# Kernel optimization log

Measured on AMD Instinct MI355X. Metric: run time of the kernel, lower is better.

Reference implementation:

```python
import jax, jax.numpy as jnp
import numpy as np

ORDER = 32


def setup_inputs() -> dict:
    key = jax.random.key(0)
    ks = jax.random.split(key, 12)
    S, N, W, OUT = 2048, 100000, ORDER * ORDER, 4 * ORDER * ORDER
    sc = lambda fan_in: 1.0 / np.sqrt(fan_in)
    return {
        "sources": jax.random.normal(ks[0], (S, 4), jnp.float32),
        "r": jax.random.normal(ks[1], (N, 2), jnp.float32),
        "W1": jax.random.normal(ks[2], (W, 4), jnp.float32) * sc(4),
        "b1": jax.random.normal(ks[3], (W,), jnp.float32) * 0.01,
        "W2": jax.random.normal(ks[4], (W, W), jnp.float32) * sc(W),
        "b2": jax.random.normal(ks[5], (W,), jnp.float32) * 0.01,
        "W3": jax.random.normal(ks[6], (W, W), jnp.float32) * sc(W),
        "b3": jax.random.normal(ks[7], (W,), jnp.float32) * 0.01,
        "W4": jax.random.normal(ks[8], (OUT, W), jnp.float32) * sc(W),
        "b4": jax.random.normal(ks[9], (OUT,), jnp.float32) * 0.01,
        "Wb": jax.random.normal(ks[10], (4,), jnp.float32) * sc(4),
        "bb": jax.random.normal(ks[11], (), jnp.float32) * 0.01,
    }


def reference(sources, r, W1, b1, W2, b2, W3, b3, W4, b4, Wb, bb):
    order = ORDER
    # hypermodel MLP (vmapped over sources == batched matmuls)
    h = jax.nn.gelu(sources @ W1.T + b1)
    h = jax.nn.gelu(h @ W2.T + b2)
    h = jax.nn.gelu(h @ W3.T + b3)
    w = h @ W4.T + b4                       # (S, 4*order^2)
    b = sources @ Wb + bb                   # (S,) scalar bias per source
    # prepare_weights: sum over sources
    wsum = jnp.sum(w, axis=0).reshape(4, order, order)
    bsum = jnp.sum(b)
    # fourier_expansion: sum_{c,i,j} w[c,i,j] * basis[c,i,j,n]
    omega = 2.0 * jnp.pi * jnp.arange(1, order + 1, dtype=r.dtype) / 10.0
    ox = omega[:, None] * r[None, :, 0]     # (order, N)
    oy = omega[:, None] * r[None, :, 1]     # (order, N)
    cx, sx = jnp.cos(ox), jnp.sin(ox)
    cy, sy = jnp.cos(oy), jnp.sin(oy)
    # basis channels: [cx*cy, sx*sy, cx*sy, sx*cy]
    xb = jnp.stack([cx, sx, cx, sx], axis=0)  # (4, order, N)
    yb = jnp.stack([cy, sy, sy, cy], axis=0)  # (4, order, N)
    summed = jnp.einsum("cij,cin,cjn->n", wsum, xb, yb)
    return bsum + summed                    # (N,)
```

## Files before the change

### kernel.cpp

```cpp
#include <hip/hip_runtime.h>
#include <math.h>

#define NSRC 2048
#define HID  1024
#define NORD 32
#define FSTR 72

typedef __bf16 bf16_t;
typedef bf16_t bf16x8 __attribute__((ext_vector_type(8)));
typedef bf16_t bf16x4 __attribute__((ext_vector_type(4)));
typedef float  f32x4  __attribute__((ext_vector_type(4)));

__device__ __forceinline__ float gelu_f(float x) {
  float u = 0.7978845608028654f * x * (1.0f + 0.044715f * x * x);
  return 0.5f * x * (1.0f + tanhf(u));
}

__global__ __launch_bounds__(256) void head_kernel(
    const float* __restrict__ sources, const float* __restrict__ W1,
    const float* __restrict__ b1, bf16_t* __restrict__ h1b,
    const float* __restrict__ W2, const float* __restrict__ W3,
    bf16_t* __restrict__ W2b, bf16_t* __restrict__ W3b,
    float* __restrict__ hsum) {
  int idx = blockIdx.x * 256 + threadIdx.x;
  if (blockIdx.x == 0) {
    for (int c = threadIdx.x; c < HID; c += 256) hsum[c] = 0.0f;
  }
  const int HALF = HID * HID / 4;
  if (idx < 2 * HALF) {
    const float* src = (idx < HALF) ? W2 : W3;
    bf16_t* dst = (idx < HALF) ? W2b : W3b;
    int j = (idx < HALF) ? idx : idx - HALF;
    float4 v = ((const float4*)src)[j];
    bf16x4 o = {(bf16_t)v.x, (bf16_t)v.y, (bf16_t)v.z, (bf16_t)v.w};
    ((bf16x4*)dst)[j] = o;
  }
  int s = idx >> 10;
  int n = idx & (HID - 1);
  float4 src4 = *(const float4*)(sources + 4 * s);
  float4 w    = *(const float4*)(W1 + 4 * n);
  float z = src4.x * w.x + src4.y * w.y + src4.z * w.z + src4.w * w.w + b1[n];
  h1b[idx] = (bf16_t)gelu_f(z);
}

template <bool WRITE_C, bool COLSUM>
__global__ __launch_bounds__(256) void gemm_bf16_mfma(
    const bf16_t* __restrict__ A, const bf16_t* __restrict__ B,
    const float* __restrict__ bias, bf16_t* __restrict__ C,
    float* __restrict__ hsum) {
  const int K = 1024, NDIM = 1024;
  __shared__ bf16_t As[2][64 * 64];
  __shared__ bf16_t Bs[2][64 * 64];
  const int tid  = threadIdx.x;
  const int wave = tid >> 6;
  const int lane = tid & 63;
  const int tm = blockIdx.y * 64;
  const int tn = blockIdx.x * 64;
  const int wm = (wave & 1) * 32;
  const int wn = (wave >> 1) * 32;

  const int row0 = tid >> 3;
  const int pc   = tid & 7;
  const int lc   = pc ^ (row0 & 7);
  const bf16_t* gA = A + (size_t)(tm + row0) * K + lc * 8;
  const bf16_t* gB = B + (size_t)(tn + row0) * K + lc * 8;

  const int col15 = lane & 15;
  const int quad  = lane >> 4;
  const int rsw   = col15 & 7;
  f32x4 acc[2][2] = {};

  bf16x8 ra0 = *(const bf16x8*)(gA);
  bf16x8 ra1 = *(const bf16x8*)(gA + (size_t)32 * K);
  bf16x8 rb0 = *(const bf16x8*)(gB);
  bf16x8 rb1 = *(const bf16x8*)(gB + (size_t)32 * K);

#define COMPUTE_TILE(b)                                                        \
  do {                                                                         \
    _Pragma("unroll")                                                          \
    for (int s = 0; s < 2; ++s) {                                              \
      const int pck = (s * 4 + quad) ^ rsw;                                    \
      bf16x8 a0 = *(const bf16x8*)(&As[b][(wm + col15) * 64 + pck * 8]);       \
      bf16x8 a1 = *(const bf16x8*)(&As[b][(wm + 16 + col15) * 64 + pck * 8]);  \
      bf16x8 b0 = *(const bf16x8*)(&Bs[b][(wn + col15) * 64 + pck * 8]);       \
      bf16x8 b1 = *(const bf16x8*)(&Bs[b][(wn + 16 + col15) * 64 + pck * 8]);  \
      acc[0][0] = __builtin_amdgcn_mfma_f32_16x16x32_bf16(a0, b0, acc[0][0], 0, 0, 0); \
      acc[0][1] = __builtin_amdgcn_mfma_f32_16x16x32_bf16(a0, b1, acc[0][1], 0, 0, 0); \
      acc[1][0] = __builtin_amdgcn_mfma_f32_16x16x32_bf16(a1, b0, acc[1][0], 0, 0, 0); \
      acc[1][1] = __builtin_amdgcn_mfma_f32_16x16x32_bf16(a1, b1, acc[1][1], 0, 0, 0); \
    }                                                                          \
  } while (0)

  for (int k0 = 0; k0 < K; k0 += 64) {
    const int buf = (k0 >> 6) & 1;
    __syncthreads();
    *(bf16x8*)(&As[buf][tid * 8])         = ra0;
    *(bf16x8*)(&As[buf][(tid + 256) * 8]) = ra1;
    *(bf16x8*)(&Bs[buf][tid * 8])         = rb0;
    *(bf16x8*)(&Bs[buf][(tid + 256) * 8]) = rb1;
    if (k0 + 64 < K) {
      ra0 = *(const bf16x8*)(gA + k0 + 64);
      ra1 = *(const bf16x8*)(gA + (size_t)32 * K + k0 + 64);
      rb0 = *(const bf16x8*)(gB + k0 + 64);
      rb1 = *(const bf16x8*)(gB + (size_t)32 * K + k0 + 64);
    }
    if (k0 > 0) COMPUTE_TILE(buf ^ 1);
  }
  __syncthreads();
  COMPUTE_TILE(1);
#undef COMPUTE_TILE

  const int rq = quad * 4;
#pragma unroll
  for (int j = 0; j < 2; ++j) {
    const int col = tn + wn + j * 16 + col15;
    const float bj = bias[col];
    float cs = 0.0f;
#pragma unroll
    for (int i = 0; i < 2; ++i) {
      const int rbase = tm + wm + i * 16 + rq;
#pragma unroll
      for (int p = 0; p < 4; ++p) {
        float v = gelu_f(acc[i][j][p] + bj);
        if (WRITE_C) C[(size_t)(rbase + p) * NDIM + col] = (bf16_t)v;
        if (COLSUM) cs += v;
      }
    }
    if (COLSUM) {
      cs += __shfl_xor(cs, 16, 64);
      cs += __shfl_xor(cs, 32, 64);
      if (lane < 16) atomicAdd(&hsum[col], cs);
    }
  }
}

__global__ __launch_bounds__(256) void gemv_kernel(
    const float* __restrict__ W4, const float* __restrict__ hsum,
    const float* __restrict__ b4, bf16_t* __restrict__ Wbig,
    const float* __restrict__ sources, const float* __restrict__ Wb,
    const float* __restrict__ bb, float* __restrict__ bsum) {
  if (blockIdx.x == 1024) {
    float a = 0.0f;
    float w0 = Wb[0], w1 = Wb[1], w2 = Wb[2], w3 = Wb[3];
    for (int s = threadIdx.x; s < NSRC; s += 256) {
      float4 src = *(const float4*)(sources + 4 * s);
      a += src.x * w0 + src.y * w1 + src.z * w2 + src.w * w3;
    }
#pragma unroll
    for (int off = 32; off; off >>= 1) a += __shfl_down(a, off, 64);
    __shared__ float wred[4];
    if ((threadIdx.x & 63) == 0) wred[threadIdx.x >> 6] = a;
    __syncthreads();
    if (threadIdx.x == 0)
      bsum[0] = wred[0] + wred[1] + wred[2] + wred[3] + (float)NSRC * bb[0];
    return;
  }
  int o = blockIdx.x * 4 + (threadIdx.x >> 6);
  int lane = threadIdx.x & 63;
  const float* row = W4 + (size_t)o * HID;
  float acc = 0.0f;
#pragma unroll
  for (int t = 0; t < 4; ++t) {
    float4 rv = *(const float4*)(row + t * 256 + lane * 4);
    float4 hv = *(const float4*)(hsum + t * 256 + lane * 4);
    acc = fmaf(rv.x, hv.x, acc);
    acc = fmaf(rv.y, hv.y, acc);
    acc = fmaf(rv.z, hv.z, acc);
    acc = fmaf(rv.w, hv.w, acc);
  }
#pragma unroll
  for (int off = 32; off; off >>= 1) acc += __shfl_down(acc, off, 64);
  if (lane == 0) {
    float val = acc + (float)NSRC * b4[o];
    int c = o >> 10, i5 = (o >> 5) & 31, j5 = o & 31;
    int m = i5 + (((c == 1) || (c == 3)) ? 32 : 0);
    int k = j5 + (((c == 1) || (c == 2)) ? 32 : 0);
    Wbig[m * 64 + k] = (bf16_t)val;
  }
}

__global__ __launch_bounds__(256) void fourier_mfma(
    const float* __restrict__ r, const bf16_t* __restrict__ Wbig,
    const float* __restrict__ bsum, float* __restrict__ out, int N) {
  __shared__ bf16_t Ws[64 * FSTR];
  __shared__ bf16_t Zs[64 * FSTR];
  __shared__ bf16_t Xs[64 * FSTR];
  const int tid  = threadIdx.x;
  const int wave = tid >> 6;
  const int lane = tid & 63;

  {
    const bf16x8* Wg = (const bf16x8*)Wbig;
    bf16x8 w0 = Wg[2 * tid], w1 = Wg[2 * tid + 1];
    int wrow = tid >> 2;
    int wcol = (tid & 3) * 16;
    *(bf16x8*)(Ws + wrow * FSTR + wcol) = w0;
    *(bf16x8*)(Ws + wrow * FSTR + wcol + 8) = w1;
  }

  {
    const int p = tid >> 2, q = tid & 3;
    int n = blockIdx.x * 64 + p;
    if (n >= N) n = N - 1;
    const float W0 = 0.6283185307179586f;
    float xw = W0 * r[2 * n], yw = W0 * r[2 * n + 1];
    float a = (float)(q + 1);
    float s1x, c1x, s4x, c4x, s1y, c1y, s4y, c4y;
    sincosf(a * xw, &s1x, &c1x);
    sincosf(4.0f * xw, &s4x, &c4x);
    sincosf(a * yw, &s1y, &c1y);
    sincosf(4.0f * yw, &s4y, &c4y);
    float cxv = c1x, sxv = s1x, cyv = c1y, syv = s1y;
#pragma unroll
    for (int t = 0; t < 8; ++t) {
      int j = q + 4 * t;
      Zs[p * FSTR + j]      = (bf16_t)cyv;
      Zs[p * FSTR + 32 + j] = (bf16_t)syv;
      Xs[p * FSTR + j]      = (bf16_t)cxv;
      Xs[p * FSTR + 32 + j] = (bf16_t)sxv;
      float tc = cxv * c4x - sxv * s4x; sxv = sxv * c4x + cxv * s4x; cxv = tc;
      tc = cyv * c4y - syv * s4y; syv = syv * c4y + cyv * s4y; cyv = tc;
    }
  }
  __syncthreads();

  const int col15 = lane & 15;
  const int quad  = lane >> 4;
  const int q8    = quad * 8;
  f32x4 G[4] = {};
#pragma unroll
  for (int kc = 0; kc < 2; ++kc) {
    bf16x8 bz = *(const bf16x8*)(Zs + (wave * 16 + col15) * FSTR + kc * 32 + q8);
#pragma unroll
    for (int mt = 0; mt < 4; ++mt) {
      bf16x8 af = *(const bf16x8*)(Ws + (mt * 16 + col15) * FSTR + kc * 32 + q8);
      G[mt] = __builtin_amdgcn_mfma_f32_16x16x32_bf16(af, bz, G[mt], 0, 0, 0);
    }
  }

  const int pt = wave * 16 + col15;
  float s = 0.0f;
#pragma unroll
  for (int mt = 0; mt < 4; ++mt) {
    bf16x4 xv = *(const bf16x4*)(Xs + pt * FSTR + mt * 16 + quad * 4);
    s += (float)xv[0] * G[mt][0] + (float)xv[1] * G[mt][1] +
         (float)xv[2] * G[mt][2] + (float)xv[3] * G[mt][3];
  }
  s += __shfl_xor(s, 16, 64);
  s += __shfl_xor(s, 32, 64);
  if (lane < 16) {
    int n2 = blockIdx.x * 64 + pt;
    if (n2 >= N) n2 = N - 1;
    out[n2] = s + bsum[0];
  }
}

extern "C" void kernel_launch(void* const* d_in, const int* in_sizes, int n_in,
                              void* d_out, int out_size, void* d_ws, size_t ws_size,
                              hipStream_t stream) {
  const float* sources = (const float*)d_in[0];
  const float* r   = (const float*)d_in[1];
  const float* W1  = (const float*)d_in[2];
  const float* b1  = (const float*)d_in[3];
  const float* W2  = (const float*)d_in[4];
  const float* b2  = (const float*)d_in[5];
  const float* W3  = (const float*)d_in[6];
  const float* b3  = (const float*)d_in[7];
  const float* W4  = (const float*)d_in[8];
  const float* b4  = (const float*)d_in[9];
  const float* Wb  = (const float*)d_in[10];
  const float* bb  = (const float*)d_in[11];
  float* out = (float*)d_out;

  char* ws = (char*)d_ws;
  bf16_t* h1b  = (bf16_t*)(ws);
  bf16_t* h2b  = (bf16_t*)(ws + (4 << 20));
  bf16_t* W2b  = (bf16_t*)(ws + (8 << 20));
  bf16_t* W3b  = (bf16_t*)(ws + (10 << 20));
  float*  hsum = (float*)(ws + (12 << 20));
  bf16_t* Wbig = (bf16_t*)(ws + (12 << 20) + 4096);
  float*  bsum = (float*)(ws + (12 << 20) + 16384);

  int N = out_size;

  head_kernel<<<NSRC * HID / 256, 256, 0, stream>>>(
      sources, W1, b1, h1b, W2, W3, W2b, W3b, hsum);
  gemm_bf16_mfma<true, false><<<dim3(HID / 64, NSRC / 64), 256, 0, stream>>>(
      h1b, W2b, b2, h2b, nullptr);
  gemm_bf16_mfma<false, true><<<dim3(HID / 64, NSRC / 64), 256, 0, stream>>>(
      h2b, W3b, b3, nullptr, hsum);
  gemv_kernel<<<1025, 256, 0, stream>>>(W4, hsum, b4, Wbig, sources, Wb, bb, bsum);
  fourier_mfma<<<(N + 63) / 64, 256, 0, stream>>>(r, Wbig, bsum, out, N);
}
```

Before: 127.9 us.

## Fuse all stages into one persistent kernel with atomic grid barriers

Merges the five launches (head, two GEMMs, GEMV, Fourier) into a single persistent kernel of 512 blocks, separated by atomic-counter grid barriers, with hsum and the barrier counter zeroed by a memset. Tile coordinates are remapped so tiles sharing rows and columns land on the same XCD, aiming for better L2 reuse. The goal is to remove launch gaps and inter-kernel tails. In exchange it relies on all 512 blocks being co-resident, which could deadlock otherwise. Later phases run grid-stride loops over fewer blocks, which may lower parallelism in the Fourier stage.

```diff
diff --git a/kernel.cpp b/kernel.cpp
--- a/kernel.cpp
+++ b/kernel.cpp
@@ -3,8 +3,9 @@
 
 #define NSRC 2048
 #define HID  1024
-#define NORD 32
 #define FSTR 72
+#define NBLK 512
+#define NTHR 256
 
 typedef __bf16 bf16_t;
 typedef bf16_t bf16x8 __attribute__((ext_vector_type(8)));
@@ -16,46 +17,26 @@
   return 0.5f * x * (1.0f + tanhf(u));
 }
 
-__global__ __launch_bounds__(256) void head_kernel(
-    const float* __restrict__ sources, const float* __restrict__ W1,
-    const float* __restrict__ b1, bf16_t* __restrict__ h1b,
-    const float* __restrict__ W2, const float* __restrict__ W3,
-    bf16_t* __restrict__ W2b, bf16_t* __restrict__ W3b,
-    float* __restrict__ hsum) {
-  int idx = blockIdx.x * 256 + threadIdx.x;
-  if (blockIdx.x == 0) {
-    for (int c = threadIdx.x; c < HID; c += 256) hsum[c] = 0.0f;
-  }
-  const int HALF = HID * HID / 4;
-  if (idx < 2 * HALF) {
-    const float* src = (idx < HALF) ? W2 : W3;
-    bf16_t* dst = (idx < HALF) ? W2b : W3b;
-    int j = (idx < HALF) ? idx : idx - HALF;
-    float4 v = ((const float4*)src)[j];
-    bf16x4 o = {(bf16_t)v.x, (bf16_t)v.y, (bf16_t)v.z, (bf16_t)v.w};
-    ((bf16x4*)dst)[j] = o;
-  }
-  int s = idx >> 10;
-  int n = idx & (HID - 1);
-  float4 src4 = *(const float4*)(sources + 4 * s);
-  float4 w    = *(const float4*)(W1 + 4 * n);
-  float z = src4.x * w.x + src4.y * w.y + src4.z * w.z + src4.w * w.w + b1[n];
-  h1b[idx] = (bf16_t)gelu_f(z);
+__device__ __forceinline__ void grid_bar(unsigned* cnt, unsigned target) {
+  __syncthreads();
+  if (threadIdx.x == 0) {
+    __hip_atomic_fetch_add(cnt, 1u, __ATOMIC_RELEASE, __HIP_MEMORY_SCOPE_AGENT);
+    while (__hip_atomic_load(cnt, __ATOMIC_RELAXED, __HIP_MEMORY_SCOPE_AGENT) < target)
+      __builtin_amdgcn_s_sleep(2);
+    (void)__hip_atomic_load(cnt, __ATOMIC_ACQUIRE, __HIP_MEMORY_SCOPE_AGENT);
+  }
+  __syncthreads();
 }
 
 template <bool WRITE_C, bool COLSUM>
-__global__ __launch_bounds__(256) void gemm_bf16_mfma(
+__device__ __forceinline__ void gemm_stage(
     const bf16_t* __restrict__ A, const bf16_t* __restrict__ B,
     const float* __restrict__ bias, bf16_t* __restrict__ C,
-    float* __restrict__ hsum) {
+    float* __restrict__ hsum, bf16_t* Asb, bf16_t* Bsb, int tm, int tn) {
   const int K = 1024, NDIM = 1024;
-  __shared__ bf16_t As[2][64 * 64];
-  __shared__ bf16_t Bs[2][64 * 64];
   const int tid  = threadIdx.x;
   const int wave = tid >> 6;
   const int lane = tid & 63;
-  const int tm = blockIdx.y * 64;
-  const int tn = blockIdx.x * 64;
   const int wm = (wave & 1) * 32;
   const int wn = (wave >> 1) * 32;
 
@@ -80,10 +61,10 @@
     _Pragma("unroll")                                                          \
     for (int s = 0; s < 2; ++s) {                                              \
       const int pck = (s * 4 + quad) ^ rsw;                                    \
-      bf16x8 a0 = *(const bf16x8*)(&As[b][(wm + col15) * 64 + pck * 8]);       \
-      bf16x8 a1 = *(const bf16x8*)(&As[b][(wm + 16 + col15) * 64 + pck * 8]);  \
-      bf16x8 b0 = *(const bf16x8*)(&Bs[b][(wn + col15) * 64 + pck * 8]);       \
-      bf16x8 b1 = *(const bf16x8*)(&Bs[b][(wn + 16 + col15) * 64 + pck * 8]);  \
+      bf16x8 a0 = *(const bf16x8*)(&Asb[(b)*4096 + (wm + col15) * 64 + pck * 8]);      \
+      bf16x8 a1 = *(const bf16x8*)(&Asb[(b)*4096 + (wm + 16 + col15) * 64 + pck * 8]); \
+      bf16x8 b0 = *(const bf16x8*)(&Bsb[(b)*4096 + (wn + col15) * 64 + pck * 8]);      \
+      bf16x8 b1 = *(const bf16x8*)(&Bsb[(b)*4096 + (wn + 16 + col15) * 64 + pck * 8]); \
       acc[0][0] = __builtin_amdgcn_mfma_f32_16x16x32_bf16(a0, b0, acc[0][0], 0, 0, 0); \
       acc[0][1] = __builtin_amdgcn_mfma_f32_16x16x32_bf16(a0, b1, acc[0][1], 0, 0, 0); \
       acc[1][0] = __builtin_amdgcn_mfma_f32_16x16x32_bf16(a1, b0, acc[1][0], 0, 0, 0); \
@@ -94,10 +75,10 @@
   for (int k0 = 0; k0 < K; k0 += 64) {
     const int buf = (k0 >> 6) & 1;
     __syncthreads();
-    *(bf16x8*)(&As[buf][tid * 8])         = ra0;
-    *(bf16x8*)(&As[buf][(tid + 256) * 8]) = ra1;
-    *(bf16x8*)(&Bs[buf][tid * 8])         = rb0;
-    *(bf16x8*)(&Bs[buf][(tid + 256) * 8]) = rb1;
+    *(bf16x8*)(&Asb[buf * 4096 + tid * 8])         = ra0;
+    *(bf16x8*)(&Asb[buf * 4096 + (tid + 256) * 8]) = ra1;
+    *(bf16x8*)(&Bsb[buf * 4096 + tid * 8])         = rb0;
+    *(bf16x8*)(&Bsb[buf * 4096 + (tid + 256) * 8]) = rb1;
     if (k0 + 64 < K) {
       ra0 = *(const bf16x8*)(gA + k0 + 64);
       ra1 = *(const bf16x8*)(gA + (size_t)32 * K + k0 + 64);
@@ -122,11 +103,11 @@
 #pragma unroll
       for (int p = 0; p < 4; ++p) {
         float v = gelu_f(acc[i][j][p] + bj);
-        if (WRITE_C) C[(size_t)(rbase + p) * NDIM + col] = (bf16_t)v;
-        if (COLSUM) cs += v;
-      }
-    }
-    if (COLSUM) {
+        if constexpr (WRITE_C) C[(size_t)(rbase + p) * NDIM + col] = (bf16_t)v;
+        if constexpr (COLSUM) cs += v;
+      }
+    }
+    if constexpr (COLSUM) {
       cs += __shfl_xor(cs, 16, 64);
       cs += __shfl_xor(cs, 32, 64);
       if (lane < 16) atomicAdd(&hsum[col], cs);
@@ -134,124 +115,175 @@
   }
 }
 
-__global__ __launch_bounds__(256) void gemv_kernel(
-    const float* __restrict__ W4, const float* __restrict__ hsum,
-    const float* __restrict__ b4, bf16_t* __restrict__ Wbig,
-    const float* __restrict__ sources, const float* __restrict__ Wb,
-    const float* __restrict__ bb, float* __restrict__ bsum) {
-  if (blockIdx.x == 1024) {
-    float a = 0.0f;
-    float w0 = Wb[0], w1 = Wb[1], w2 = Wb[2], w3 = Wb[3];
-    for (int s = threadIdx.x; s < NSRC; s += 256) {
-      float4 src = *(const float4*)(sources + 4 * s);
-      a += src.x * w0 + src.y * w1 + src.z * w2 + src.w * w3;
-    }
-#pragma unroll
-    for (int off = 32; off; off >>= 1) a += __shfl_down(a, off, 64);
-    __shared__ float wred[4];
-    if ((threadIdx.x & 63) == 0) wred[threadIdx.x >> 6] = a;
-    __syncthreads();
-    if (threadIdx.x == 0)
-      bsum[0] = wred[0] + wred[1] + wred[2] + wred[3] + (float)NSRC * bb[0];
-    return;
-  }
-  int o = blockIdx.x * 4 + (threadIdx.x >> 6);
-  int lane = threadIdx.x & 63;
-  const float* row = W4 + (size_t)o * HID;
-  float acc = 0.0f;
-#pragma unroll
-  for (int t = 0; t < 4; ++t) {
-    float4 rv = *(const float4*)(row + t * 256 + lane * 4);
-    float4 hv = *(const float4*)(hsum + t * 256 + lane * 4);
-    acc = fmaf(rv.x, hv.x, acc);
-    acc = fmaf(rv.y, hv.y, acc);
-    acc = fmaf(rv.z, hv.z, acc);
-    acc = fmaf(rv.w, hv.w, acc);
-  }
-#pragma unroll
-  for (int off = 32; off; off >>= 1) acc += __shfl_down(acc, off, 64);
-  if (lane == 0) {
-    float val = acc + (float)NSRC * b4[o];
-    int c = o >> 10, i5 = (o >> 5) & 31, j5 = o & 31;
-    int m = i5 + (((c == 1) || (c == 3)) ? 32 : 0);
-    int k = j5 + (((c == 1) || (c == 2)) ? 32 : 0);
-    Wbig[m * 64 + k] = (bf16_t)val;
-  }
-}
-
-__global__ __launch_bounds__(256) void fourier_mfma(
-    const float* __restrict__ r, const bf16_t* __restrict__ Wbig,
-    const float* __restrict__ bsum, float* __restrict__ out, int N) {
-  __shared__ bf16_t Ws[64 * FSTR];
-  __shared__ bf16_t Zs[64 * FSTR];
-  __shared__ bf16_t Xs[64 * FSTR];
-  const int tid  = threadIdx.x;
-  const int wave = tid >> 6;
-  const int lane = tid & 63;
+__global__ __launch_bounds__(NTHR, 2) void fused_all(
+    const float* __restrict__ sources, const float* __restrict__ r,
+    const float* __restrict__ W1, const float* __restrict__ b1,
+    const float* __restrict__ W2, const float* __restrict__ b2,
+    const float* __restrict__ W3, const float* __restrict__ b3,
+    const float* __restrict__ W4, const float* __restrict__ b4,
+    const float* __restrict__ Wb, const float* __restrict__ bb,
+    bf16_t* __restrict__ h1b, bf16_t* __restrict__ h2b,
+    bf16_t* __restrict__ W2b, bf16_t* __restrict__ W3b,
+    float* __restrict__ hsum, bf16_t* __restrict__ Wbig,
+    float* __restrict__ bsum, unsigned* __restrict__ bar,
+    float* __restrict__ out, int N) {
+  extern __shared__ __align__(16) unsigned char smem[];
+  bf16_t* Asb = (bf16_t*)smem;
+  bf16_t* Bsb = (bf16_t*)(smem + 16384);
+  const int tid = threadIdx.x;
 
   {
-    const bf16x8* Wg = (const bf16x8*)Wbig;
-    bf16x8 w0 = Wg[2 * tid], w1 = Wg[2 * tid + 1];
-    int wrow = tid >> 2;
-    int wcol = (tid & 3) * 16;
-    *(bf16x8*)(Ws + wrow * FSTR + wcol) = w0;
-    *(bf16x8*)(Ws + wrow * FSTR + wcol + 8) = w1;
-  }
-
+    const int HALF = HID * HID / 4;
+    for (int idx = blockIdx.x * NTHR + tid; idx < NSRC * HID; idx += NBLK * NTHR) {
+      if (idx < 2 * HALF) {
+        const float* src = (idx < HALF) ? W2 : W3;
+        bf16_t* dst = (idx < HALF) ? W2b : W3b;
+        int j = (idx < HALF) ? idx : idx - HALF;
+        float4 v = ((const float4*)src)[j];
+        bf16x4 o = {(bf16_t)v.x, (bf16_t)v.y, (bf16_t)v.z, (bf16_t)v.w};
+        ((bf16x4*)dst)[j] = o;
+      }
+      int s = idx >> 10;
+      int n = idx & (HID - 1);
+      float4 src4 = *(const float4*)(sources + 4 * s);
+      float4 w    = *(const float4*)(W1 + 4 * n);
+      float z = src4.x * w.x + src4.y * w.y + src4.z * w.z + src4.w * w.w + b1[n];
+      h1b[idx] = (bf16_t)gelu_f(z);
+    }
+  }
+  grid_bar(bar, NBLK * 1);
+
+  int tm, tn;
   {
-    const int p = tid >> 2, q = tid & 3;
-    int n = blockIdx.x * 64 + p;
-    if (n >= N) n = N - 1;
-    const float W0 = 0.6283185307179586f;
-    float xw = W0 * r[2 * n], yw = W0 * r[2 * n + 1];
-    float a = (float)(q + 1);
-    float s1x, c1x, s4x, c4x, s1y, c1y, s4y, c4y;
-    sincosf(a * xw, &s1x, &c1x);
-    sincosf(4.0f * xw, &s4x, &c4x);
-    sincosf(a * yw, &s1y, &c1y);
-    sincosf(4.0f * yw, &s4y, &c4y);
-    float cxv = c1x, sxv = s1x, cyv = c1y, syv = s1y;
-#pragma unroll
-    for (int t = 0; t < 8; ++t) {
-      int j = q + 4 * t;
-      Zs[p * FSTR + j]      = (bf16_t)cyv;
-      Zs[p * FSTR + 32 + j] = (bf16_t)syv;
-      Xs[p * FSTR + j]      = (bf16_t)cxv;
-      Xs[p * FSTR + 32 + j] = (bf16_t)sxv;
-      float tc = cxv * c4x - sxv * s4x; sxv = sxv * c4x + cxv * s4x; cxv = tc;
-      tc = cyv * c4y - syv * s4y; syv = syv * c4y + cyv * s4y; cyv = tc;
-    }
-  }
-  __syncthreads();
-
-  const int col15 = lane & 15;
-  const int quad  = lane >> 4;
-  const int q8    = quad * 8;
-  f32x4 G[4] = {};
-#pragma unroll
-  for (int kc = 0; kc < 2; ++kc) {
-    bf16x8 bz = *(const bf16x8*)(Zs + (wave * 16 + col15) * FSTR + kc * 32 + q8);
-#pragma unroll
-    for (int mt = 0; mt < 4; ++mt) {
-      bf16x8 af = *(const bf16x8*)(Ws + (mt * 16 + col15) * FSTR + kc * 32 + q8);
-      G[mt] = __builtin_amdgcn_mfma_f32_16x16x32_bf16(af, bz, G[mt], 0, 0, 0);
-    }
-  }
-
-  const int pt = wave * 16 + col15;
-  float s = 0.0f;
-#pragma unroll
-  for (int mt = 0; mt < 4; ++mt) {
-    bf16x4 xv = *(const bf16x4*)(Xs + pt * FSTR + mt * 16 + quad * 4);
-    s += (float)xv[0] * G[mt][0] + (float)xv[1] * G[mt][1] +
-         (float)xv[2] * G[mt][2] + (float)xv[3] * G[mt][3];
-  }
-  s += __shfl_xor(s, 16, 64);
-  s += __shfl_xor(s, 32, 64);
-  if (lane < 16) {
-    int n2 = blockIdx.x * 64 + pt;
-    if (n2 >= N) n2 = N - 1;
-    out[n2] = s + bsum[0];
+    const int b = blockIdx.x;
+    const int xcd = b & 7, j = b >> 3;
+    tm = ((xcd >> 1) * 8 + (j >> 3)) * 64;
+    tn = ((xcd & 1) * 8 + (j & 7)) * 64;
+  }
+
+  gemm_stage<true, false>(h1b, W2b, b2, h2b, nullptr, Asb, Bsb, tm, tn);
+  grid_bar(bar, NBLK * 2);
+
+  gemm_stage<false, true>(h2b, W3b, b3, nullptr, hsum, Asb, Bsb, tm, tn);
+  grid_bar(bar, NBLK * 3);
+
+  for (int vb = blockIdx.x; vb <= 1024; vb += NBLK) {
+    if (vb == 1024) {
+      float a = 0.0f;
+      float w0 = Wb[0], w1 = Wb[1], w2 = Wb[2], w3 = Wb[3];
+      for (int s = tid; s < NSRC; s += NTHR) {
+        float4 src = *(const float4*)(sources + 4 * s);
+        a += src.x * w0 + src.y * w1 + src.z * w2 + src.w * w3;
+      }
+#pragma unroll
+      for (int off = 32; off; off >>= 1) a += __shfl_down(a, off, 64);
+      float* wred = (float*)smem;
+      if ((tid & 63) == 0) wred[tid >> 6] = a;
+      __syncthreads();
+      if (tid == 0)
+        bsum[0] = wred[0] + wred[1] + wred[2] + wred[3] + (float)NSRC * bb[0];
+    } else {
+      int o = vb * 4 + (tid >> 6);
+      int lane = tid & 63;
+      const float* row = W4 + (size_t)o * HID;
+      float acc = 0.0f;
+#pragma unroll
+      for (int t = 0; t < 4; ++t) {
+        float4 rv = *(const float4*)(row + t * 256 + lane * 4);
+        float4 hv = *(const float4*)(hsum + t * 256 + lane * 4);
+        acc = fmaf(rv.x, hv.x, acc);
+        acc = fmaf(rv.y, hv.y, acc);
+        acc = fmaf(rv.z, hv.z, acc);
+        acc = fmaf(rv.w, hv.w, acc);
+      }
+#pragma unroll
+      for (int off = 32; off; off >>= 1) acc += __shfl_down(acc, off, 64);
+      if (lane == 0) {
+        float val = acc + (float)NSRC * b4[o];
+        int c = o >> 10, i5 = (o >> 5) & 31, j5 = o & 31;
+        int m = i5 + (((c == 1) || (c == 3)) ? 32 : 0);
+        int k = j5 + (((c == 1) || (c == 2)) ? 32 : 0);
+        Wbig[m * 64 + k] = (bf16_t)val;
+      }
+    }
+  }
+  grid_bar(bar, NBLK * 4);
+
+  {
+    bf16_t* Ws = (bf16_t*)smem;
+    bf16_t* Zs = Ws + 64 * FSTR;
+    bf16_t* Xs = Zs + 64 * FSTR;
+    const int wave = tid >> 6;
+    const int lane = tid & 63;
+    const int nF = (N + 63) >> 6;
+    bool wloaded = false;
+    for (int vb = blockIdx.x; vb < nF; vb += NBLK) {
+      __syncthreads();
+      if (!wloaded) {
+        const bf16x8* Wg = (const bf16x8*)Wbig;
+        bf16x8 w0 = Wg[2 * tid], w1 = Wg[2 * tid + 1];
+        int wrow = tid >> 2;
+        int wcol = (tid & 3) * 16;
+        *(bf16x8*)(Ws + wrow * FSTR + wcol) = w0;
+        *(bf16x8*)(Ws + wrow * FSTR + wcol + 8) = w1;
+        wloaded = true;
+      }
+      {
+        const int p = tid >> 2, q = tid & 3;
+        int n = vb * 64 + p;
+        if (n >= N) n = N - 1;
+        const float W0 = 0.6283185307179586f;
+        float xw = W0 * r[2 * n], yw = W0 * r[2 * n + 1];
+        float a = (float)(q + 1);
+        float s1x, c1x, s4x, c4x, s1y, c1y, s4y, c4y;
+        sincosf(a * xw, &s1x, &c1x);
+        sincosf(4.0f * xw, &s4x, &c4x);
+        sincosf(a * yw, &s1y, &c1y);
+        sincosf(4.0f * yw, &s4y, &c4y);
+        float cxv = c1x, sxv = s1x, cyv = c1y, syv = s1y;
+#pragma unroll
+        for (int t = 0; t < 8; ++t) {
+          int j = q + 4 * t;
+          Zs[p * FSTR + j]      = (bf16_t)cyv;
+          Zs[p * FSTR + 32 + j] = (bf16_t)syv;
+          Xs[p * FSTR + j]      = (bf16_t)cxv;
+          Xs[p * FSTR + 32 + j] = (bf16_t)sxv;
+          float tc = cxv * c4x - sxv * s4x; sxv = sxv * c4x + cxv * s4x; cxv = tc;
+          tc = cyv * c4y - syv * s4y; syv = syv * c4y + cyv * s4y; cyv = tc;
+        }
+      }
+      __syncthreads();
+
+      const int col15 = lane & 15;
+      const int quad  = lane >> 4;
+      const int q8    = quad * 8;
+      f32x4 G[4] = {};
+#pragma unroll
+      for (int kc = 0; kc < 2; ++kc) {
+        bf16x8 bz = *(const bf16x8*)(Zs + (wave * 16 + col15) * FSTR + kc * 32 + q8);
+#pragma unroll
+        for (int mt = 0; mt < 4; ++mt) {
+          bf16x8 af = *(const bf16x8*)(Ws + (mt * 16 + col15) * FSTR + kc * 32 + q8);
+          G[mt] = __builtin_amdgcn_mfma_f32_16x16x32_bf16(af, bz, G[mt], 0, 0, 0);
+        }
+      }
+
+      const int pt = wave * 16 + col15;
+      float s = 0.0f;
+#pragma unroll
+      for (int mt = 0; mt < 4; ++mt) {
+        bf16x4 xv = *(const bf16x4*)(Xs + pt * FSTR + mt * 16 + quad * 4);
+        s += (float)xv[0] * G[mt][0] + (float)xv[1] * G[mt][1] +
+             (float)xv[2] * G[mt][2] + (float)xv[3] * G[mt][3];
+      }
+      s += __shfl_xor(s, 16, 64);
+      s += __shfl_xor(s, 32, 64);
+      if (lane < 16) {
+        int n2 = vb * 64 + pt;
+        if (n2 >= N) n2 = N - 1;
+        out[n2] = s + bsum[0];
+      }
+    }
   }
 }
 
@@ -277,18 +309,17 @@
   bf16_t* h2b  = (bf16_t*)(ws + (4 << 20));
   bf16_t* W2b  = (bf16_t*)(ws + (8 << 20));
   bf16_t* W3b  = (bf16_t*)(ws + (10 << 20));
-  float*  hsum = (float*)(ws + (12 << 20));
-  bf16_t* Wbig = (bf16_t*)(ws + (12 << 20) + 4096);
-  float*  bsum = (float*)(ws + (12 << 20) + 16384);
+  char*   ctl  = ws + (12 << 20);
+  float*  hsum = (float*)(ctl);
+  bf16_t* Wbig = (bf16_t*)(ctl + 4096);
+  float*  bsum = (float*)(ctl + 12288);
+  unsigned* bar = (unsigned*)(ctl + 12292);
 
   int N = out_size;
 
-  head_kernel<<<NSRC * HID / 256, 256, 0, stream>>>(
-      sources, W1, b1, h1b, W2, W3, W2b, W3b, hsum);
-  gemm_bf16_mfma<true, false><<<dim3(HID / 64, NSRC / 64), 256, 0, stream>>>(
-      h1b, W2b, b2, h2b, nullptr);
-  gemm_bf16_mfma<false, true><<<dim3(HID / 64, NSRC / 64), 256, 0, stream>>>(
-      h2b, W3b, b3, nullptr, hsum);
-  gemv_kernel<<<1025, 256, 0, stream>>>(W4, hsum, b4, Wbig, sources, Wb, bb, bsum);
-  fourier_mfma<<<(N + 63) / 64, 256, 0, stream>>>(r, Wbig, bsum, out, N);
-}
+  hipMemsetAsync(ctl, 0, 16384, stream);
+
+  fused_all<<<NBLK, NTHR, 32768, stream>>>(
+      sources, r, W1, b1, W2, b2, W3, b3, W4, b4, Wb, bb,
+      h1b, h2b, W2b, W3b, hsum, Wbig, bsum, bar, out, N);
+}
```

Measured after the change: 247.2 us. 1.93x slower.

## Fuse weight bf16 conversion into GEMM loads and use hardware sin/cos

Applied to the files above, without the earlier changes.

The separate pass that converts W2 and W3 to bf16 is removed; the GEMMs now load fp32 B tiles and convert them to bf16 while staging into shared memory. The head kernel now handles four outputs per thread with packed 64-bit stores, hsum is zeroed with a memset, and the Fourier kernel replaces sincosf with fract plus the hardware sin/cos builtins. Each GEMM block now reads twice the bytes for B, and the same weights are re-read by 32 row blocks, which adds global traffic. The hardware sin/cos is also less accurate.

```diff
diff --git a/kernel.cpp b/kernel.cpp
--- a/kernel.cpp
+++ b/kernel.cpp
@@ -10,42 +10,43 @@
 typedef bf16_t bf16x8 __attribute__((ext_vector_type(8)));
 typedef bf16_t bf16x4 __attribute__((ext_vector_type(4)));
 typedef float  f32x4  __attribute__((ext_vector_type(4)));
+typedef unsigned long long u64;
 
 __device__ __forceinline__ float gelu_f(float x) {
   float u = 0.7978845608028654f * x * (1.0f + 0.044715f * x * x);
   return 0.5f * x * (1.0f + tanhf(u));
 }
 
+__device__ __forceinline__ bf16x8 cvt8(f32x4 a, f32x4 b) {
+  bf16x8 o = {(bf16_t)a[0], (bf16_t)a[1], (bf16_t)a[2], (bf16_t)a[3],
+              (bf16_t)b[0], (bf16_t)b[1], (bf16_t)b[2], (bf16_t)b[3]};
+  return o;
+}
+
 __global__ __launch_bounds__(256) void head_kernel(
     const float* __restrict__ sources, const float* __restrict__ W1,
-    const float* __restrict__ b1, bf16_t* __restrict__ h1b,
-    const float* __restrict__ W2, const float* __restrict__ W3,
-    bf16_t* __restrict__ W2b, bf16_t* __restrict__ W3b,
-    float* __restrict__ hsum) {
-  int idx = blockIdx.x * 256 + threadIdx.x;
-  if (blockIdx.x == 0) {
-    for (int c = threadIdx.x; c < HID; c += 256) hsum[c] = 0.0f;
-  }
-  const int HALF = HID * HID / 4;
-  if (idx < 2 * HALF) {
-    const float* src = (idx < HALF) ? W2 : W3;
-    bf16_t* dst = (idx < HALF) ? W2b : W3b;
-    int j = (idx < HALF) ? idx : idx - HALF;
-    float4 v = ((const float4*)src)[j];
-    bf16x4 o = {(bf16_t)v.x, (bf16_t)v.y, (bf16_t)v.z, (bf16_t)v.w};
-    ((bf16x4*)dst)[j] = o;
-  }
-  int s = idx >> 10;
-  int n = idx & (HID - 1);
+    const float* __restrict__ b1, bf16_t* __restrict__ h1b) {
+  int i4 = blockIdx.x * 256 + threadIdx.x;
+  int s = i4 >> 8;
+  int n0 = (i4 & 255) << 2;
   float4 src4 = *(const float4*)(sources + 4 * s);
-  float4 w    = *(const float4*)(W1 + 4 * n);
-  float z = src4.x * w.x + src4.y * w.y + src4.z * w.z + src4.w * w.w + b1[n];
-  h1b[idx] = (bf16_t)gelu_f(z);
+  float4 bv   = *(const float4*)(b1 + n0);
+  float barr[4] = {bv.x, bv.y, bv.z, bv.w};
+  union { unsigned short h[4]; u64 u; } pk;
+#pragma unroll
+  for (int jj = 0; jj < 4; ++jj) {
+    float4 w = *(const float4*)(W1 + 4 * (n0 + jj));
+    float z = src4.x * w.x + src4.y * w.y + src4.z * w.z + src4.w * w.w +
+              barr[jj];
+    union { bf16_t b; unsigned short s16; } cv; cv.b = (bf16_t)gelu_f(z);
+    pk.h[jj] = cv.s16;
+  }
+  *(u64*)(h1b + (size_t)i4 * 4) = pk.u;
 }
 
 template <bool WRITE_C, bool COLSUM>
 __global__ __launch_bounds__(256) void gemm_bf16_mfma(
-    const bf16_t* __restrict__ A, const bf16_t* __restrict__ B,
+    const bf16_t* __restrict__ A, const float* __restrict__ B,
     const float* __restrict__ bias, bf16_t* __restrict__ C,
     float* __restrict__ hsum) {
   const int K = 1024, NDIM = 1024;
@@ -63,7 +64,7 @@
   const int pc   = tid & 7;
   const int lc   = pc ^ (row0 & 7);
   const bf16_t* gA = A + (size_t)(tm + row0) * K + lc * 8;
-  const bf16_t* gB = B + (size_t)(tn + row0) * K + lc * 8;
+  const float*  gB = B + (size_t)(tn + row0) * K + lc * 8;
 
   const int col15 = lane & 15;
   const int quad  = lane >> 4;
@@ -72,8 +73,10 @@
 
   bf16x8 ra0 = *(const bf16x8*)(gA);
   bf16x8 ra1 = *(const bf16x8*)(gA + (size_t)32 * K);
-  bf16x8 rb0 = *(const bf16x8*)(gB);
-  bf16x8 rb1 = *(const bf16x8*)(gB + (size_t)32 * K);
+  f32x4 rb00 = *(const f32x4*)(gB);
+  f32x4 rb01 = *(const f32x4*)(gB + 4);
+  f32x4 rb10 = *(const f32x4*)(gB + (size_t)32 * K);
+  f32x4 rb11 = *(const f32x4*)(gB + (size_t)32 * K + 4);
 
 #define COMPUTE_TILE(b)                                                        \
   do {                                                                         \
@@ -96,13 +99,15 @@
     __syncthreads();
     *(bf16x8*)(&As[buf][tid * 8])         = ra0;
     *(bf16x8*)(&As[buf][(tid + 256) * 8]) = ra1;
-    *(bf16x8*)(&Bs[buf][tid * 8])         = rb0;
-    *(bf16x8*)(&Bs[buf][(tid + 256) * 8]) = rb1;
+    *(bf16x8*)(&Bs[buf][tid * 8])         = cvt8(rb00, rb01);
+    *(bf16x8*)(&Bs[buf][(tid + 256) * 8]) = cvt8(rb10, rb11);
     if (k0 + 64 < K) {
-      ra0 = *(const bf16x8*)(gA + k0 + 64);
-      ra1 = *(const bf16x8*)(gA + (size_t)32 * K + k0 + 64);
-      rb0 = *(const bf16x8*)(gB + k0 + 64);
-      rb1 = *(const bf16x8*)(gB + (size_t)32 * K + k0 + 64);
+      ra0  = *(const bf16x8*)(gA + k0 + 64);
+      ra1  = *(const bf16x8*)(gA + (size_t)32 * K + k0 + 64);
+      rb00 = *(const f32x4*)(gB + k0 + 64);
+      rb01 = *(const f32x4*)(gB + k0 + 68);
+      rb10 = *(const f32x4*)(gB + (size_t)32 * K + k0 + 64);
+      rb11 = *(const f32x4*)(gB + (size_t)32 * K + k0 + 68);
     }
     if (k0 > 0) COMPUTE_TILE(buf ^ 1);
   }
@@ -202,14 +207,16 @@
     const int p = tid >> 2, q = tid & 3;
     int n = blockIdx.x * 64 + p;
     if (n >= N) n = N - 1;
-    const float W0 = 0.6283185307179586f;
-    float xw = W0 * r[2 * n], yw = W0 * r[2 * n + 1];
+    float rx = r[2 * n] * 0.1f, ry = r[2 * n + 1] * 0.1f;
     float a = (float)(q + 1);
-    float s1x, c1x, s4x, c4x, s1y, c1y, s4y, c4y;
-    sincosf(a * xw, &s1x, &c1x);
-    sincosf(4.0f * xw, &s4x, &c4x);
-    sincosf(a * yw, &s1y, &c1y);
-    sincosf(4.0f * yw, &s4y, &c4y);
+    float f1x = __builtin_amdgcn_fractf(a * rx);
+    float f4x = __builtin_amdgcn_fractf(4.0f * rx);
+    float f1y = __builtin_amdgcn_fractf(a * ry);
+    float f4y = __builtin_amdgcn_fractf(4.0f * ry);
+    float s1x = __builtin_amdgcn_sinf(f1x), c1x = __builtin_amdgcn_cosf(f1x);
+    float s4x = __builtin_amdgcn_sinf(f4x), c4x = __builtin_amdgcn_cosf(f4x);
+    float s1y = __builtin_amdgcn_sinf(f1y), c1y = __builtin_amdgcn_cosf(f1y);
+    float s4y = __builtin_amdgcn_sinf(f4y), c4y = __builtin_amdgcn_cosf(f4y);
     float cxv = c1x, sxv = s1x, cyv = c1y, syv = s1y;
 #pragma unroll
     for (int t = 0; t < 8; ++t) {
@@ -275,20 +282,19 @@
   char* ws = (char*)d_ws;
   bf16_t* h1b  = (bf16_t*)(ws);
   bf16_t* h2b  = (bf16_t*)(ws + (4 << 20));
-  bf16_t* W2b  = (bf16_t*)(ws + (8 << 20));
-  bf16_t* W3b  = (bf16_t*)(ws + (10 << 20));
-  float*  hsum = (float*)(ws + (12 << 20));
-  bf16_t* Wbig = (bf16_t*)(ws + (12 << 20) + 4096);
-  float*  bsum = (float*)(ws + (12 << 20) + 16384);
+  float*  hsum = (float*)(ws + (8 << 20));
+  bf16_t* Wbig = (bf16_t*)(ws + (8 << 20) + 4096);
+  float*  bsum = (float*)(ws + (8 << 20) + 16384);
 
   int N = out_size;
 
-  head_kernel<<<NSRC * HID / 256, 256, 0, stream>>>(
-      sources, W1, b1, h1b, W2, W3, W2b, W3b, hsum);
+  hipMemsetAsync(hsum, 0, 4096, stream);
+
+  head_kernel<<<NSRC * HID / 1024, 256, 0, stream>>>(sources, W1, b1, h1b);
   gemm_bf16_mfma<true, false><<<dim3(HID / 64, NSRC / 64), 256, 0, stream>>>(
-      h1b, W2b, b2, h2b, nullptr);
+      h1b, W2, b2, h2b, nullptr);
   gemm_bf16_mfma<false, true><<<dim3(HID / 64, NSRC / 64), 256, 0, stream>>>(
-      h2b, W3b, b3, nullptr, hsum);
+      h2b, W3, b3, nullptr, hsum);
   gemv_kernel<<<1025, 256, 0, stream>>>(W4, hsum, b4, Wbig, sources, Wb, bb, bsum);
   fourier_mfma<<<(N + 63) / 64, 256, 0, stream>>>(r, Wbig, bsum, out, N);
 }
```

Measured after the change: 134.2 us. 5.0% more time.
